# Kernel optimization log

Measured on AMD Instinct MI355X. Metric: run time of the kernel, lower is better.

The kernel has to match this reference:

```python
import jax, jax.numpy as jnp
import numpy as np

EMBED_DIM = 256
NUM_EMB = 4096
COMMIT = 0.25


def setup_inputs() -> dict:
    key = jax.random.key(0)
    k1, k2 = jax.random.split(key)
    inputs = jax.random.normal(k1, (32, 256, 32, 32), dtype=jnp.float32)
    # torch init is uniform(-3, 3); use same scale
    embeddings = jax.random.uniform(k2, (NUM_EMB, EMBED_DIM), dtype=jnp.float32,
                                    minval=-3.0, maxval=3.0)
    return {"inputs": inputs, "embeddings": embeddings, "is_training": 1}


def reference(inputs, embeddings, is_training):
    # inputs: [N, C, H, W] with C == EMBED_DIM; embeddings: [K, C]
    x = jnp.transpose(inputs, (0, 3, 2, 1))          # [N, W, H, C] (torch transpose(1,3))
    flat = x.reshape(-1, EMBED_DIM)                   # [T, C]
    distances = (jnp.sum(flat * flat, axis=1, keepdims=True)
                 - 2.0 * flat @ embeddings.T
                 + jnp.sum(embeddings * embeddings, axis=1)[None, :])
    idx_flat = jnp.argmax(-distances, axis=1)         # [T]
    encodings = jax.nn.one_hot(idx_flat, NUM_EMB, dtype=jnp.float32)  # [T, K]
    encoding_indices = idx_flat.reshape(x.shape[:-1])  # [N, W, H]
    quantized = embeddings[encoding_indices]            # [N, W, H, C]

    e_latent_loss = jnp.mean((jax.lax.stop_gradient(quantized) - x) ** 2)
    q_latent_loss = jnp.mean((quantized - jax.lax.stop_gradient(x)) ** 2)
    loss = q_latent_loss + COMMIT * e_latent_loss

    quantized_st = x + jax.lax.stop_gradient(quantized - x)

    avg_probs = jnp.mean(encodings, axis=0)             # [K]
    perplexity = jnp.exp(-jnp.sum(avg_probs * jnp.log(avg_probs + 1e-10)))

    quantize_out = jnp.transpose(quantized_st, (0, 3, 2, 1))  # back to [N, C, H, W]
    return quantize_out, loss, perplexity, encodings, encoding_indices, distances
```

## Files before the change

### kernel.cpp

```cpp
#include <hip/hip_runtime.h>
#include <math.h>

constexpr int NB = 32, HH = 32, WW = 32, CD = 256, NK = 4096;
constexpr int T_ = NB * WW * HH;
constexpr long long NQ = (long long)NB * CD * HH * WW;
constexpr long long OFF_LOSS = NQ;
constexpr long long OFF_PERP = NQ + 1;
constexpr long long OFF_ENC  = NQ + 2;
constexpr long long ENC_SZ   = (long long)T_ * NK;
constexpr long long OFF_IDX  = OFF_ENC + ENC_SZ;
constexpr long long OFF_DIST = OFF_IDX + T_;
constexpr long long SCR_FLAT = OFF_ENC + 2;
constexpr long long SCR_PVAL = SCR_FLAT + (long long)T_ * CD;
constexpr long long SCR_PIDX = SCR_PVAL + (long long)T_ * 32;

#define TID ((int)threadIdx.x)

__global__ __launch_bounds__(256) void k_transpose(const float* __restrict__ in,
                                                   float* __restrict__ flat) {
  __shared__ float t[256][33];
  int b = blockIdx.x, n = b >> 5, h = b & 31;
  int w = TID & 31, c8 = TID >> 5;
  const float* src = in + (long long)n * 262144 + h * 32;
#pragma unroll
  for (int p = 0; p < 32; ++p) {
    int c = p * 8 + c8;
    t[c][w] = src[c * 1024 + w];
  }
  __syncthreads();
  float* dst = flat + ((long long)n * 1024 + h) * 256;
#pragma unroll
  for (int w2 = 0; w2 < 32; ++w2) dst[w2 * 8192 + TID] = t[TID][w2];
}

__global__ __launch_bounds__(256) void k_rowsq(const float* __restrict__ src,
                                               float* __restrict__ dst, int nrows) {
  int row = blockIdx.x * 4 + (TID >> 6);
  if (row >= nrows) return;
  int lane = TID & 63;
  float4 v = *(const float4*)(src + (long long)row * 256 + lane * 4);
  float s = v.x * v.x + v.y * v.y + v.z * v.z + v.w * v.w;
#pragma unroll
  for (int o = 32; o; o >>= 1) s += __shfl_down(s, o);
  if (lane == 0) dst[row] = s;
}

__global__ __launch_bounds__(256) void k_gemm(const float* __restrict__ A,
                                              const float* __restrict__ B,
                                              const float* __restrict__ xsq,
                                              const float* __restrict__ esq,
                                              float* __restrict__ dist,
                                              float* __restrict__ pval,
                                              int* __restrict__ pidx) {
  __shared__ float As[16][132];
  __shared__ float Bs[16][132];
  int tid = TID;
  int bm = blockIdx.x >> 5, bn = blockIdx.x & 31;
  int tn = tid & 15, tm = tid >> 4;
  int lr = tid >> 2, lk = tid & 3;
  const float* Ag = A + (long long)bm * 128 * 256 + lr * 256 + lk * 4;
  const float* Bg = B + (long long)bn * 128 * 256 + lr * 256 + lk * 4;

  float acc[2][4][2][4] = {};
  for (int kt = 0; kt < 16; ++kt) {
    float4 a0 = *(const float4*)(Ag + kt * 16);
    float4 a1 = *(const float4*)(Ag + 64 * 256 + kt * 16);
    float4 b0 = *(const float4*)(Bg + kt * 16);
    float4 b1 = *(const float4*)(Bg + 64 * 256 + kt * 16);
    __syncthreads();
    As[lk * 4 + 0][lr] = a0.x; As[lk * 4 + 1][lr] = a0.y;
    As[lk * 4 + 2][lr] = a0.z; As[lk * 4 + 3][lr] = a0.w;
    As[lk * 4 + 0][lr + 64] = a1.x; As[lk * 4 + 1][lr + 64] = a1.y;
    As[lk * 4 + 2][lr + 64] = a1.z; As[lk * 4 + 3][lr + 64] = a1.w;
    Bs[lk * 4 + 0][lr] = b0.x; Bs[lk * 4 + 1][lr] = b0.y;
    Bs[lk * 4 + 2][lr] = b0.z; Bs[lk * 4 + 3][lr] = b0.w;
    Bs[lk * 4 + 0][lr + 64] = b1.x; Bs[lk * 4 + 1][lr + 64] = b1.y;
    Bs[lk * 4 + 2][lr + 64] = b1.z; Bs[lk * 4 + 3][lr + 64] = b1.w;
    __syncthreads();
#pragma unroll
    for (int kk = 0; kk < 16; ++kk) {
      float4 av0 = *(const float4*)&As[kk][tm * 4];
      float4 av1 = *(const float4*)&As[kk][64 + tm * 4];
      float4 bv0 = *(const float4*)&Bs[kk][tn * 4];
      float4 bv1 = *(const float4*)&Bs[kk][64 + tn * 4];
      const float* ap0 = &av0.x; const float* ap1 = &av1.x;
      const float* bp0 = &bv0.x; const float* bp1 = &bv1.x;
#pragma unroll
      for (int i = 0; i < 4; ++i)
#pragma unroll
        for (int j = 0; j < 4; ++j) {
          acc[0][i][0][j] = fmaf(ap0[i], bp0[j], acc[0][i][0][j]);
          acc[0][i][1][j] = fmaf(ap0[i], bp1[j], acc[0][i][1][j]);
          acc[1][i][0][j] = fmaf(ap1[i], bp0[j], acc[1][i][0][j]);
          acc[1][i][1][j] = fmaf(ap1[i], bp1[j], acc[1][i][1][j]);
        }
    }
  }
  float4 es0 = *(const float4*)(esq + bn * 128 + tn * 4);
  float4 es1 = *(const float4*)(esq + bn * 128 + 64 + tn * 4);
  const float* ep0 = &es0.x; const float* ep1 = &es1.x;
#pragma unroll
  for (int hh = 0; hh < 2; ++hh)
#pragma unroll
    for (int i = 0; i < 4; ++i) {
      int row = bm * 128 + hh * 64 + tm * 4 + i;
      float xs = xsq[row];
      float dv[8];
#pragma unroll
      for (int j = 0; j < 4; ++j) {
        dv[j]     = xs - 2.0f * acc[hh][i][0][j] + ep0[j];
        dv[4 + j] = xs - 2.0f * acc[hh][i][1][j] + ep1[j];
      }
      float bv = 3.4e38f; int bc = 0;
#pragma unroll
      for (int g = 0; g < 2; ++g)
#pragma unroll
        for (int j = 0; j < 4; ++j) {
          float v = dv[g * 4 + j];
          int c = g * 64 + tn * 4 + j;
          if (v < bv) { bv = v; bc = c; }
        }
      float* drow = dist + (long long)row * 4096 + bn * 128;
      *(float2*)(drow + tn * 4)          = make_float2(dv[0], dv[1]);
      *(float2*)(drow + tn * 4 + 2)      = make_float2(dv[2], dv[3]);
      *(float2*)(drow + 64 + tn * 4)     = make_float2(dv[4], dv[5]);
      *(float2*)(drow + 64 + tn * 4 + 2) = make_float2(dv[6], dv[7]);
#pragma unroll
      for (int m = 1; m < 16; m <<= 1) {
        float ov = __shfl_xor(bv, m);
        int oc = __shfl_xor(bc, m);
        if (ov < bv || (ov == bv && oc < bc)) { bv = ov; bc = oc; }
      }
      if (tn == 0) {
        pval[(long long)row * 32 + bn] = bv;
        pidx[(long long)row * 32 + bn] = bn * 128 + bc;
      }
    }
}

__global__ __launch_bounds__(256) void k_argmin(const float* __restrict__ pval,
                                                const int* __restrict__ pidx,
                                                int* __restrict__ idxArr,
                                                float* __restrict__ outIdx,
                                                int* __restrict__ hist) {
  int t = blockIdx.x * 256 + TID;
  float bv = 3.4e38f; int bc = 0;
#pragma unroll
  for (int b = 0; b < 32; ++b) {
    float v = pval[(long long)t * 32 + b];
    if (v < bv) { bv = v; bc = pidx[(long long)t * 32 + b]; }
  }
  idxArr[t] = bc;
  outIdx[t] = (float)bc;
  atomicAdd(&hist[bc], 1);
}

__global__ __launch_bounds__(256) void k_scatter(const int* __restrict__ idxArr,
                                                 float* __restrict__ enc) {
  int t = blockIdx.x * 256 + TID;
  enc[(long long)t * 4096 + idxArr[t]] = 1.0f;
}

__global__ __launch_bounds__(256) void k_quant(const float* __restrict__ in,
                                               const float* __restrict__ emb,
                                               const int* __restrict__ idxArr,
                                               float* __restrict__ outQ,
                                               float* __restrict__ lossAcc) {
  __shared__ float q[32][257];
  __shared__ float ls[4];
  int b = blockIdx.x, n = b >> 5, h = b & 31;
  for (int w = 0; w < 32; ++w) {
    int id = idxArr[(n * 32 + w) * 32 + h];
    q[w][TID] = emb[(long long)id * 256 + TID];
  }
  __syncthreads();
  float sum = 0.f;
  int w = TID & 31, c8 = TID >> 5;
  const float* xin = in + (long long)n * 262144 + h * 32;
  float* xout = outQ + (long long)n * 262144 + h * 32;
#pragma unroll
  for (int p = 0; p < 32; ++p) {
    int c = p * 8 + c8;
    float qa = q[w][c];
    float xv = xin[c * 1024 + w];
    float d = qa - xv;
    sum += d * d;
    xout[c * 1024 + w] = qa;
  }
#pragma unroll
  for (int o = 32; o; o >>= 1) sum += __shfl_down(sum, o);
  if ((TID & 63) == 0) ls[TID >> 6] = sum;
  __syncthreads();
  if (TID == 0) atomicAdd(lossAcc, ls[0] + ls[1] + ls[2] + ls[3]);
}

__global__ __launch_bounds__(256) void k_final(const int* __restrict__ hist,
                                               const float* __restrict__ lossAcc,
                                               float* __restrict__ outLoss,
                                               float* __restrict__ outPerp) {
  __shared__ float ls[4];
  float s = 0.f;
  for (int k = TID; k < 4096; k += 256) {
    float p = (float)hist[k] * (1.0f / 32768.0f);
    s += p * logf(p + 1e-10f);
  }
#pragma unroll
  for (int o = 32; o; o >>= 1) s += __shfl_down(s, o);
  if ((TID & 63) == 0) ls[TID >> 6] = s;
  __syncthreads();
  if (TID == 0) {
    *outLoss = lossAcc[0] * (1.25f / 8388608.0f);
    *outPerp = expf(-(ls[0] + ls[1] + ls[2] + ls[3]));
  }
}

extern "C" void kernel_launch(void* const* d_in, const int* in_sizes, int n_in,
                              void* d_out, int out_size, void* d_ws, size_t ws_size,
                              hipStream_t stream) {
  const float* inputs = (const float*)d_in[0];
  const float* emb = (const float*)d_in[1];
  float* out = (float*)d_out;
  float* ws = (float*)d_ws;

  float* lossAcc = ws;
  int* hist = (int*)(ws + 64);
  float* xsq = ws + 8192;
  float* esq = ws + 40960;
  int* idxArr = (int*)(ws + 45056);

  float* flat = out + SCR_FLAT;
  float* pval = out + SCR_PVAL;
  int* pidx = (int*)(out + SCR_PIDX);
  float* dist = out + OFF_DIST;
  float* enc = out + OFF_ENC;

  hipMemsetAsync(d_ws, 0, 8192 * 4, stream);
  k_transpose<<<1024, 256, 0, stream>>>(inputs, flat);
  k_rowsq<<<8192, 256, 0, stream>>>(flat, xsq, 32768);
  k_rowsq<<<1024, 256, 0, stream>>>(emb, esq, 4096);
  k_gemm<<<8192, 256, 0, stream>>>(flat, emb, xsq, esq, dist, pval, pidx);
  k_argmin<<<128, 256, 0, stream>>>(pval, pidx, idxArr, out + OFF_IDX, hist);
  hipMemsetAsync(enc, 0, (size_t)ENC_SZ * 4, stream);
  k_scatter<<<128, 256, 0, stream>>>(idxArr, enc);
  k_quant<<<1024, 256, 0, stream>>>(inputs, emb, idxArr, out, lossAcc);
  k_final<<<1, 256, 0, stream>>>(hist, lossAcc, out + OFF_LOSS, out + OFF_PERP);
}
```

Measured before the change: 1.881 ms.

## Use split-fp16 MFMA for distance GEMM with exact fp32 fixup of near ties

Packs inputs and codebook into hi/lo fp16 pairs with a swizzled layout and computes the distance GEMM with 3-term MFMA (hi*hi + hi*lo + lo*hi), loading tiles directly into LDS. Argmin tracks the second-best distance and flags rows whose margin is small; a fixup kernel recomputes those rows exactly in fp32 to preserve argmin correctness. The one-hot encoding is written in a single pass instead of a memset plus scatter. The distances output now carries reduced-precision error, and the fixup cost depends on how many rows get flagged.

```diff
diff --git a/kernel.cpp b/kernel.cpp
--- a/kernel.cpp
+++ b/kernel.cpp
@@ -10,14 +10,23 @@
 constexpr long long ENC_SZ   = (long long)T_ * NK;
 constexpr long long OFF_IDX  = OFF_ENC + ENC_SZ;
 constexpr long long OFF_DIST = OFF_IDX + T_;
-constexpr long long SCR_FLAT = OFF_ENC + 2;
-constexpr long long SCR_PVAL = SCR_FLAT + (long long)T_ * CD;
-constexpr long long SCR_PIDX = SCR_PVAL + (long long)T_ * 32;
+constexpr long long SCR0    = 8388612;
+constexpr long long O_APK   = SCR0;
+constexpr long long O_EPK   = SCR0 + 8388608;
+constexpr long long O_FLAT  = O_EPK + 1048576;
+constexpr long long O_PVAL  = O_FLAT + 8388608;
+constexpr long long O_PIDX  = O_PVAL + 2097152;
+constexpr long long O_FLAGS = O_PIDX + 2097152;
 
 #define TID ((int)threadIdx.x)
 
-__global__ __launch_bounds__(256) void k_transpose(const float* __restrict__ in,
-                                                   float* __restrict__ flat) {
+typedef _Float16 f16x8 __attribute__((ext_vector_type(8)));
+typedef _Float16 f16x4v __attribute__((ext_vector_type(4)));
+typedef float f32x4 __attribute__((ext_vector_type(4)));
+
+__global__ __launch_bounds__(256) void k_pack_x(const float* __restrict__ in,
+                                                float* __restrict__ flat,
+                                                char* __restrict__ apk) {
   __shared__ float t[256][33];
   int b = blockIdx.x, n = b >> 5, h = b & 31;
   int w = TID & 31, c8 = TID >> 5;
@@ -28,9 +37,39 @@
     t[c][w] = src[c * 1024 + w];
   }
   __syncthreads();
-  float* dst = flat + ((long long)n * 1024 + h) * 256;
-#pragma unroll
-  for (int w2 = 0; w2 < 32; ++w2) dst[w2 * 8192 + TID] = t[TID][w2];
+  int c = TID;
+  long long trow = (long long)n * 1024 + h;
+#pragma unroll
+  for (int w2 = 0; w2 < 32; ++w2) {
+    long long ti = trow + w2 * 32;
+    float v = t[c][w2];
+    flat[ti * 256 + c] = v;
+    _Float16 hi = (_Float16)v;
+    _Float16 lo = (_Float16)(v - (float)hi);
+    char* pb = apk + ti * 1024 + ((c >> 5) << 7) + ((c & 31) << 1);
+    *(_Float16*)pb = hi;
+    *(_Float16*)(pb + 64) = lo;
+  }
+}
+
+__global__ __launch_bounds__(256) void k_pack_e(const float* __restrict__ emb,
+                                                char* __restrict__ epk,
+                                                float* __restrict__ esq) {
+  int row = blockIdx.x * 4 + (TID >> 6);
+  int l = TID & 63;
+  float4 v = *(const float4*)(emb + (long long)row * 256 + l * 4);
+  f16x4v hi, lo;
+  hi[0] = (_Float16)v.x; lo[0] = (_Float16)(v.x - (float)hi[0]);
+  hi[1] = (_Float16)v.y; lo[1] = (_Float16)(v.y - (float)hi[1]);
+  hi[2] = (_Float16)v.z; lo[2] = (_Float16)(v.z - (float)hi[2]);
+  hi[3] = (_Float16)v.w; lo[3] = (_Float16)(v.w - (float)hi[3]);
+  char* pb = epk + (long long)row * 1024 + ((l >> 3) << 7) + ((l & 7) << 3);
+  *(f16x4v*)pb = hi;
+  *(f16x4v*)(pb + 64) = lo;
+  float s = v.x * v.x + v.y * v.y + v.z * v.z + v.w * v.w;
+#pragma unroll
+  for (int o = 32; o; o >>= 1) s += __shfl_down(s, o);
+  if (l == 0) esq[row] = s;
 }
 
 __global__ __launch_bounds__(256) void k_rowsq(const float* __restrict__ src,
@@ -45,120 +84,184 @@
   if (lane == 0) dst[row] = s;
 }
 
-__global__ __launch_bounds__(256) void k_gemm(const float* __restrict__ A,
-                                              const float* __restrict__ B,
+__global__ __launch_bounds__(256) void k_gemm(const char* __restrict__ apk,
+                                              const char* __restrict__ epk,
                                               const float* __restrict__ xsq,
                                               const float* __restrict__ esq,
                                               float* __restrict__ dist,
                                               float* __restrict__ pval,
                                               int* __restrict__ pidx) {
-  __shared__ float As[16][132];
-  __shared__ float Bs[16][132];
-  int tid = TID;
+  __shared__ char As[16384];
+  __shared__ char Bs[16384];
   int bm = blockIdx.x >> 5, bn = blockIdx.x & 31;
-  int tn = tid & 15, tm = tid >> 4;
-  int lr = tid >> 2, lk = tid & 3;
-  const float* Ag = A + (long long)bm * 128 * 256 + lr * 256 + lk * 4;
-  const float* Bg = B + (long long)bn * 128 * 256 + lr * 256 + lk * 4;
-
-  float acc[2][4][2][4] = {};
-  for (int kt = 0; kt < 16; ++kt) {
-    float4 a0 = *(const float4*)(Ag + kt * 16);
-    float4 a1 = *(const float4*)(Ag + 64 * 256 + kt * 16);
-    float4 b0 = *(const float4*)(Bg + kt * 16);
-    float4 b1 = *(const float4*)(Bg + 64 * 256 + kt * 16);
-    __syncthreads();
-    As[lk * 4 + 0][lr] = a0.x; As[lk * 4 + 1][lr] = a0.y;
-    As[lk * 4 + 2][lr] = a0.z; As[lk * 4 + 3][lr] = a0.w;
-    As[lk * 4 + 0][lr + 64] = a1.x; As[lk * 4 + 1][lr + 64] = a1.y;
-    As[lk * 4 + 2][lr + 64] = a1.z; As[lk * 4 + 3][lr + 64] = a1.w;
-    Bs[lk * 4 + 0][lr] = b0.x; Bs[lk * 4 + 1][lr] = b0.y;
-    Bs[lk * 4 + 2][lr] = b0.z; Bs[lk * 4 + 3][lr] = b0.w;
-    Bs[lk * 4 + 0][lr + 64] = b1.x; Bs[lk * 4 + 1][lr + 64] = b1.y;
-    Bs[lk * 4 + 2][lr + 64] = b1.z; Bs[lk * 4 + 3][lr + 64] = b1.w;
-    __syncthreads();
-#pragma unroll
-    for (int kk = 0; kk < 16; ++kk) {
-      float4 av0 = *(const float4*)&As[kk][tm * 4];
-      float4 av1 = *(const float4*)&As[kk][64 + tm * 4];
-      float4 bv0 = *(const float4*)&Bs[kk][tn * 4];
-      float4 bv1 = *(const float4*)&Bs[kk][64 + tn * 4];
-      const float* ap0 = &av0.x; const float* ap1 = &av1.x;
-      const float* bp0 = &bv0.x; const float* bp1 = &bv1.x;
-#pragma unroll
-      for (int i = 0; i < 4; ++i)
-#pragma unroll
-        for (int j = 0; j < 4; ++j) {
-          acc[0][i][0][j] = fmaf(ap0[i], bp0[j], acc[0][i][0][j]);
-          acc[0][i][1][j] = fmaf(ap0[i], bp1[j], acc[0][i][1][j]);
-          acc[1][i][0][j] = fmaf(ap1[i], bp0[j], acc[1][i][0][j]);
-          acc[1][i][1][j] = fmaf(ap1[i], bp1[j], acc[1][i][1][j]);
-        }
-    }
-  }
-  float4 es0 = *(const float4*)(esq + bn * 128 + tn * 4);
-  float4 es1 = *(const float4*)(esq + bn * 128 + 64 + tn * 4);
-  const float* ep0 = &es0.x; const float* ep1 = &es1.x;
-#pragma unroll
-  for (int hh = 0; hh < 2; ++hh)
-#pragma unroll
-    for (int i = 0; i < 4; ++i) {
-      int row = bm * 128 + hh * 64 + tm * 4 + i;
-      float xs = xsq[row];
-      float dv[8];
-#pragma unroll
-      for (int j = 0; j < 4; ++j) {
-        dv[j]     = xs - 2.0f * acc[hh][i][0][j] + ep0[j];
-        dv[4 + j] = xs - 2.0f * acc[hh][i][1][j] + ep1[j];
-      }
+  int wid = TID >> 6, l = TID & 63;
+  int wm = wid >> 1, wn = wid & 1;
+  int kg = l >> 4;
+
+  f32x4 acc[4][4];
+#pragma unroll
+  for (int i = 0; i < 4; ++i)
+#pragma unroll
+    for (int j = 0; j < 4; ++j) acc[i][j] = (f32x4){0.f, 0.f, 0.f, 0.f};
+
+  const char* srcBase = (wid < 2) ? (apk + (long long)bm * 128 * 1024)
+                                  : (epk + (long long)bn * 128 * 1024);
+  char* ldsBase = (wid < 2) ? As : Bs;
+  int rpart = (wid & 1) * 64;
+  int chunk = (l & 7) ^ ((l >> 3) & 7);
+
+  for (int kt = 0; kt < 8; ++kt) {
+#pragma unroll
+    for (int j = 0; j < 8; ++j) {
+      int rl = rpart + j * 8 + (l >> 3);
+      const char* src = srcBase + (long long)rl * 1024 + kt * 128 + chunk * 16;
+      char* dst = ldsBase + (rpart + j * 8) * 128;
+      __builtin_amdgcn_global_load_lds(
+          (const __attribute__((address_space(1))) void*)src,
+          (__attribute__((address_space(3))) void*)dst, 16, 0, 0);
+    }
+    __syncthreads();
+    f16x8 ah[4], al[4], bh[4], bl[4];
+#pragma unroll
+    for (int mf = 0; mf < 4; ++mf) {
+      int r = wm * 64 + mf * 16 + (l & 15);
+      ah[mf] = *(const f16x8*)(As + r * 128 + ((kg ^ (r & 7)) << 4));
+      al[mf] = *(const f16x8*)(As + r * 128 + (((kg + 4) ^ (r & 7)) << 4));
+    }
+#pragma unroll
+    for (int nf = 0; nf < 4; ++nf) {
+      int r = wn * 64 + nf * 16 + (l & 15);
+      bh[nf] = *(const f16x8*)(Bs + r * 128 + ((kg ^ (r & 7)) << 4));
+      bl[nf] = *(const f16x8*)(Bs + r * 128 + (((kg + 4) ^ (r & 7)) << 4));
+    }
+#pragma unroll
+    for (int mf = 0; mf < 4; ++mf)
+#pragma unroll
+      for (int nf = 0; nf < 4; ++nf) {
+        acc[mf][nf] = __builtin_amdgcn_mfma_f32_16x16x32_f16(ah[mf], bh[nf], acc[mf][nf], 0, 0, 0);
+        acc[mf][nf] = __builtin_amdgcn_mfma_f32_16x16x32_f16(ah[mf], bl[nf], acc[mf][nf], 0, 0, 0);
+        acc[mf][nf] = __builtin_amdgcn_mfma_f32_16x16x32_f16(al[mf], bh[nf], acc[mf][nf], 0, 0, 0);
+      }
+    __syncthreads();
+  }
+
+  float es[4];
+#pragma unroll
+  for (int nf = 0; nf < 4; ++nf) es[nf] = esq[bn * 128 + wn * 64 + nf * 16 + (l & 15)];
+  int rowbase = bm * 128 + wm * 64;
+  long long pblk = bn * 2 + wn;
+#pragma unroll
+  for (int mf = 0; mf < 4; ++mf) {
+    float4 x4 = *(const float4*)(xsq + rowbase + mf * 16 + kg * 4);
+    float xr[4] = {x4.x, x4.y, x4.z, x4.w};
+#pragma unroll
+    for (int r = 0; r < 4; ++r) {
+      int row = rowbase + mf * 16 + kg * 4 + r;
+      float xs = xr[r];
       float bv = 3.4e38f; int bc = 0;
 #pragma unroll
-      for (int g = 0; g < 2; ++g)
-#pragma unroll
-        for (int j = 0; j < 4; ++j) {
-          float v = dv[g * 4 + j];
-          int c = g * 64 + tn * 4 + j;
-          if (v < bv) { bv = v; bc = c; }
-        }
-      float* drow = dist + (long long)row * 4096 + bn * 128;
-      *(float2*)(drow + tn * 4)          = make_float2(dv[0], dv[1]);
-      *(float2*)(drow + tn * 4 + 2)      = make_float2(dv[2], dv[3]);
-      *(float2*)(drow + 64 + tn * 4)     = make_float2(dv[4], dv[5]);
-      *(float2*)(drow + 64 + tn * 4 + 2) = make_float2(dv[6], dv[7]);
+      for (int nf = 0; nf < 4; ++nf) {
+        float v = xs - 2.0f * acc[mf][nf][r] + es[nf];
+        dist[(long long)row * 4096 + bn * 128 + wn * 64 + nf * 16 + (l & 15)] = v;
+        if (v < bv) { bv = v; bc = nf; }
+      }
+      int col = bn * 128 + wn * 64 + bc * 16 + (l & 15);
 #pragma unroll
       for (int m = 1; m < 16; m <<= 1) {
         float ov = __shfl_xor(bv, m);
-        int oc = __shfl_xor(bc, m);
-        if (ov < bv || (ov == bv && oc < bc)) { bv = ov; bc = oc; }
-      }
-      if (tn == 0) {
-        pval[(long long)row * 32 + bn] = bv;
-        pidx[(long long)row * 32 + bn] = bn * 128 + bc;
-      }
-    }
+        int oc = __shfl_xor(col, m);
+        if (ov < bv || (ov == bv && oc < col)) { bv = ov; col = oc; }
+      }
+      if ((l & 15) == 0) {
+        pval[pblk * 32768 + row] = bv;
+        pidx[pblk * 32768 + row] = col;
+      }
+    }
+  }
 }
 
 __global__ __launch_bounds__(256) void k_argmin(const float* __restrict__ pval,
                                                 const int* __restrict__ pidx,
                                                 int* __restrict__ idxArr,
-                                                float* __restrict__ outIdx,
-                                                int* __restrict__ hist) {
+                                                int* __restrict__ flags,
+                                                int* __restrict__ nflag) {
   int t = blockIdx.x * 256 + TID;
-  float bv = 3.4e38f; int bc = 0;
-#pragma unroll
-  for (int b = 0; b < 32; ++b) {
-    float v = pval[(long long)t * 32 + b];
-    if (v < bv) { bv = v; bc = pidx[(long long)t * 32 + b]; }
+  float bv = 3.4e38f, sec = 3.4e38f; int bc = 0;
+#pragma unroll
+  for (int b = 0; b < 64; ++b) {
+    float v = pval[(long long)b * 32768 + t];
+    if (v < bv) { sec = bv; bv = v; bc = pidx[(long long)b * 32768 + t]; }
+    else if (v < sec) sec = v;
   }
   idxArr[t] = bc;
-  outIdx[t] = (float)bc;
-  atomicAdd(&hist[bc], 1);
-}
-
-__global__ __launch_bounds__(256) void k_scatter(const int* __restrict__ idxArr,
-                                                 float* __restrict__ enc) {
+  if (sec - bv < 0.125f) {
+    int p = atomicAdd(nflag, 1);
+    flags[p] = t;
+  }
+}
+
+__global__ __launch_bounds__(256) void k_fixup(const float* __restrict__ flat,
+                                               const float* __restrict__ emb,
+                                               const float* __restrict__ xsq,
+                                               const float* __restrict__ esq,
+                                               const int* __restrict__ flags,
+                                               const int* __restrict__ nflag,
+                                               int* __restrict__ idxArr) {
+  __shared__ float xrow[256];
+  __shared__ float rv[256];
+  __shared__ int rk[256];
+  int nf = *nflag;
+  for (int f = blockIdx.x; f < nf; f += 256) {
+    __syncthreads();
+    int t = flags[f];
+    xrow[TID] = flat[(long long)t * 256 + TID];
+    __syncthreads();
+    float xs = xsq[t];
+    float bv = 3.4e38f; int bk = 1 << 30;
+    for (int j = 0; j < 16; ++j) {
+      int k = j * 256 + TID;
+      const float* er = emb + (long long)k * 256;
+      float dot = 0.f;
+      for (int c = 0; c < 256; ++c) dot = fmaf(xrow[c], er[c], dot);
+      float v = xs - 2.0f * dot + esq[k];
+      if (v < bv || (v == bv && k < bk)) { bv = v; bk = k; }
+    }
+    rv[TID] = bv; rk[TID] = bk;
+    __syncthreads();
+    for (int s = 128; s; s >>= 1) {
+      if (TID < s) {
+        float ov = rv[TID + s]; int ok = rk[TID + s];
+        if (ov < rv[TID] || (ov == rv[TID] && ok < rk[TID])) { rv[TID] = ov; rk[TID] = ok; }
+      }
+      __syncthreads();
+    }
+    if (TID == 0) idxArr[t] = rk[0];
+  }
+}
+
+__global__ __launch_bounds__(256) void k_hist(const int* __restrict__ idxArr,
+                                              float* __restrict__ outIdx,
+                                              int* __restrict__ hist) {
   int t = blockIdx.x * 256 + TID;
-  enc[(long long)t * 4096 + idxArr[t]] = 1.0f;
+  int id = idxArr[t];
+  outIdx[t] = (float)id;
+  atomicAdd(&hist[id], 1);
+}
+
+__global__ __launch_bounds__(256) void k_onehot(const int* __restrict__ idxArr,
+                                                float* __restrict__ enc) {
+  int t = blockIdx.x * 4 + (TID >> 6);
+  int lane = TID & 63;
+  int id = idxArr[t];
+  float* row = enc + (long long)t * 4096;
+#pragma unroll
+  for (int j = 0; j < 16; ++j) {
+    int pos = j * 256 + lane * 4;
+    float4 z = make_float4(0.f, 0.f, 0.f, 0.f);
+    int d = id - pos;
+    if (d >= 0 && d < 4) ((float*)&z)[d] = 1.0f;
+    *(float4*)(row + pos) = z;
+  }
 }
 
 __global__ __launch_bounds__(256) void k_quant(const float* __restrict__ in,
@@ -223,25 +326,30 @@
   float* ws = (float*)d_ws;
 
   float* lossAcc = ws;
+  int* nflag = (int*)(ws + 1);
   int* hist = (int*)(ws + 64);
   float* xsq = ws + 8192;
   float* esq = ws + 40960;
   int* idxArr = (int*)(ws + 45056);
 
-  float* flat = out + SCR_FLAT;
-  float* pval = out + SCR_PVAL;
-  int* pidx = (int*)(out + SCR_PIDX);
+  char* apk = (char*)(out + O_APK);
+  char* epk = (char*)(out + O_EPK);
+  float* flat = out + O_FLAT;
+  float* pval = out + O_PVAL;
+  int* pidx = (int*)(out + O_PIDX);
+  int* flags = (int*)(out + O_FLAGS);
   float* dist = out + OFF_DIST;
   float* enc = out + OFF_ENC;
 
-  hipMemsetAsync(d_ws, 0, 8192 * 4, stream);
-  k_transpose<<<1024, 256, 0, stream>>>(inputs, flat);
+  hipMemsetAsync(d_ws, 0, 32768, stream);
+  k_pack_x<<<1024, 256, 0, stream>>>(inputs, flat, apk);
+  k_pack_e<<<1024, 256, 0, stream>>>(emb, epk, esq);
   k_rowsq<<<8192, 256, 0, stream>>>(flat, xsq, 32768);
-  k_rowsq<<<1024, 256, 0, stream>>>(emb, esq, 4096);
-  k_gemm<<<8192, 256, 0, stream>>>(flat, emb, xsq, esq, dist, pval, pidx);
-  k_argmin<<<128, 256, 0, stream>>>(pval, pidx, idxArr, out + OFF_IDX, hist);
-  hipMemsetAsync(enc, 0, (size_t)ENC_SZ * 4, stream);
-  k_scatter<<<128, 256, 0, stream>>>(idxArr, enc);
+  k_gemm<<<8192, 256, 0, stream>>>(apk, epk, xsq, esq, dist, pval, pidx);
+  k_argmin<<<128, 256, 0, stream>>>(pval, pidx, idxArr, flags, nflag);
+  k_fixup<<<256, 256, 0, stream>>>(flat, emb, xsq, esq, flags, nflag, idxArr);
+  k_hist<<<128, 256, 0, stream>>>(idxArr, out + OFF_IDX, hist);
+  k_onehot<<<8192, 256, 0, stream>>>(idxArr, enc);
   k_quant<<<1024, 256, 0, stream>>>(inputs, emb, idxArr, out, lossAcc);
   k_final<<<1, 256, 0, stream>>>(hist, lossAcc, out + OFF_LOSS, out + OFF_PERP);
 }
```

After: 1.742 ms. 7.4% less time.
